# Kernel tuning notes

Hardware: AMD Instinct MI355X
Metric: run time of the kernel (lower is better)

The kernel has to match this reference:

```python
import jax, jax.numpy as jnp
import numpy as np
from jax import lax


def _maxpool_nchw(x, k):
    # Non-overlapping kxk max pool over the last two dims (NCHW).
    return lax.reduce_window(x, -jnp.inf, lax.max,
                             window_dimensions=(1, 1, k, k),
                             window_strides=(1, 1, k, k),
                             padding='VALID')


def setup_inputs() -> dict:
    key = jax.random.key(0)
    k1, k2, k3, k4, k5 = jax.random.split(key, 5)
    B = 16
    return {
        'input_tensor1': jax.random.normal(k1, (B, 128, 48, 48), jnp.float32),
        'input_tensor2': jax.random.normal(k2, (B, 64, 96, 96), jnp.float32),
        'input_tensor3': jax.random.normal(k3, (B, 32, 192, 192), jnp.float32),
        'input_tensor4': jax.random.normal(k4, (B, 16, 384, 384), jnp.float32),
        'pure_ff': jax.random.normal(k5, (B, 256, 24, 24), jnp.float32),
    }


def reference(input_tensor1, input_tensor2, input_tensor3, input_tensor4, pure_ff):
    # and then max-pools. Pooling is per-channel, so this equals pooling once
    # and tiling the pooled result along the channel axis -- same math,
    # without materializing the redundant concat intermediates.
    x1 = jnp.tile(_maxpool_nchw(input_tensor1, 2), (1, 2, 1, 1))   # [B,256,24,24]
    x2 = jnp.tile(_maxpool_nchw(input_tensor2, 4), (1, 4, 1, 1))   # [B,256,24,24]
    x3 = jnp.tile(_maxpool_nchw(input_tensor3, 8), (1, 8, 1, 1))   # [B,256,24,24]
    x4 = jnp.tile(_maxpool_nchw(input_tensor4, 16), (1, 16, 1, 1)) # [B,256,24,24]
    return jax.nn.relu(x1 + x2 + x3 + x4 + pure_ff)
```

## Files before the change

### kernel.cpp

```cpp
#include <hip/hip_runtime.h>
#include <math.h>


namespace {

__device__ __forceinline__ float fmax4(const float4 v) {
  return fmaxf(fmaxf(v.x, v.y), fmaxf(v.z, v.w));
}

__device__ __forceinline__ float4 max4(const float4 a, const float4 b) {
  float4 r;
  r.x = fmaxf(a.x, b.x); r.y = fmaxf(a.y, b.y);
  r.z = fmaxf(a.z, b.z); r.w = fmaxf(a.w, b.w);
  return r;
}

__global__ __launch_bounds__(256, 3) void fused_block(const float* __restrict__ x1,
                                                      const float* __restrict__ x2,
                                                      const float* __restrict__ x3,
                                                      const float* __restrict__ x4,
                                                      const float* __restrict__ ff,
                                                      float* __restrict__ out) {
  __shared__ float s1t[4 * 128];
  __shared__ float s2t[4 * 64];
  __shared__ float s3t[4 * 32];
  __shared__ float s4t[4 * 16];

  const int blk  = blockIdx.x;
  const int b    = blk / 144;
  const int rem  = blk % 144;
  const int oh   = rem / 6;
  const int quad = rem % 6;
  const int tid  = threadIdx.x;


  const size_t o = (size_t)b * 147456 + (size_t)tid * 576 + (size_t)oh * 24 + quad * 4;
  const float4 f = *reinterpret_cast<const float4*>(ff + o);

  const int chA = tid >> 1, pidA = tid & 1;
  const float* pA = x1 + (size_t)b * 294912 + (size_t)chA * 2304
                       + oh * 96 + quad * 8 + pidA * 4;
  const float4 a0 = *reinterpret_cast<const float4*>(pA);
  const float4 a1 = *reinterpret_cast<const float4*>(pA + 48);

  const int chB = tid >> 2, owB = tid & 3;
  const float* pB = x2 + (size_t)b * 589824 + (size_t)chB * 9216
                       + oh * 384 + quad * 16 + owB * 4;
  float4 bv[4];
#pragma unroll
  for (int r = 0; r < 4; ++r) bv[r] = *reinterpret_cast<const float4*>(pB + r * 96);

  const int chC = tid >> 3, owC = (tid >> 1) & 3, hf = tid & 1;
  const float* pC = x3 + (size_t)b * 1179648 + (size_t)chC * 36864
                       + oh * 1536 + quad * 32 + owC * 8 + hf * 4;
  float4 cv[8];
#pragma unroll
  for (int r = 0; r < 8; ++r) cv[r] = *reinterpret_cast<const float4*>(pC + r * 192);

  const int chD = tid >> 4, owD = (tid >> 2) & 3, q = tid & 3;
  const float* pD = x4 + (size_t)b * 2359296 + (size_t)chD * 147456
                       + oh * 6144 + quad * 64 + owD * 16 + q * 4;
  float4 dv[16];
#pragma unroll
  for (int r = 0; r < 16; ++r) dv[r] = *reinterpret_cast<const float4*>(pD + r * 384);


  s1t[(pidA * 2) * 128 + chA]     = fmaxf(fmaxf(a0.x, a0.y), fmaxf(a1.x, a1.y));
  s1t[(pidA * 2 + 1) * 128 + chA] = fmaxf(fmaxf(a0.z, a0.w), fmaxf(a1.z, a1.w));

  {
    const float4 u = max4(max4(bv[0], bv[1]), max4(bv[2], bv[3]));
    s2t[owB * 64 + chB] = fmax4(u);
  }

  {
    const float4 u0 = max4(cv[0], cv[1]), u1 = max4(cv[2], cv[3]);
    const float4 u2 = max4(cv[4], cv[5]), u3 = max4(cv[6], cv[7]);
    float m = fmax4(max4(max4(u0, u1), max4(u2, u3)));
    m = fmaxf(m, __shfl_xor(m, 1));
    if (hf == 0) s3t[owC * 32 + chC] = m;
  }

  {
    float4 t[8];
#pragma unroll
    for (int r = 0; r < 8; ++r) t[r] = max4(dv[r], dv[r + 8]);
    const float4 u0 = max4(t[0], t[1]), u1 = max4(t[2], t[3]);
    const float4 u2 = max4(t[4], t[5]), u3 = max4(t[6], t[7]);
    float m = fmax4(max4(max4(u0, u1), max4(u2, u3)));
    m = fmaxf(m, __shfl_xor(m, 1));
    m = fmaxf(m, __shfl_xor(m, 2));
    if (q == 0) s4t[owD * 16 + chD] = m;
  }

  __syncthreads();

  {
    const int c1 = tid & 127, c2 = tid & 63, c3 = tid & 31, c4 = tid & 15;
    float4 r;
    r.x = fmaxf(s1t[0 * 128 + c1] + s2t[0 * 64 + c2] + s3t[0 * 32 + c3] + s4t[0 * 16 + c4] + f.x, 0.0f);
    r.y = fmaxf(s1t[1 * 128 + c1] + s2t[1 * 64 + c2] + s3t[1 * 32 + c3] + s4t[1 * 16 + c4] + f.y, 0.0f);
    r.z = fmaxf(s1t[2 * 128 + c1] + s2t[2 * 64 + c2] + s3t[2 * 32 + c3] + s4t[2 * 16 + c4] + f.z, 0.0f);
    r.w = fmaxf(s1t[3 * 128 + c1] + s2t[3 * 64 + c2] + s3t[3 * 32 + c3] + s4t[3 * 16 + c4] + f.w, 0.0f);
    *reinterpret_cast<float4*>(out + o) = r;
  }
}

}

extern "C" void kernel_launch(void* const* d_in, const int* in_sizes, int n_in,
                              void* d_out, int out_size, void* d_ws, size_t ws_size,
                              hipStream_t stream) {
  const float* x1 = (const float*)d_in[0];
  const float* x2 = (const float*)d_in[1];
  const float* x3 = (const float*)d_in[2];
  const float* x4 = (const float*)d_in[3];
  const float* ff = (const float*)d_in[4];
  float* out = (float*)d_out;
  (void)d_ws; (void)ws_size; (void)in_sizes; (void)n_in; (void)out_size;

  fused_block<<<2304, 256, 0, stream>>>(x1, x2, x3, x4, ff, out);
}
```

Baseline: 316.5 us.

## Use persistent blocks with double-buffered direct global-to-LDS DMA loads

Replaces the one-shot 2304-block kernel with 256 persistent 512-thread blocks. Each block walks 18 tiles, prefetching the next tile's inputs into a double-buffered LDS region with global_load_lds while it reduces the current tile. The aim is to overlap memory latency with compute and to avoid staging loads through registers. In exchange, tiles shrink to two output columns, so output stores become scalar and poorly coalesced. Occupancy also drops to one large block per CU, with extra barriers and manual vmcnt waits.

```diff
diff --git a/kernel.cpp b/kernel.cpp
--- a/kernel.cpp
+++ b/kernel.cpp
@@ -1,13 +1,37 @@
 #include <hip/hip_runtime.h>
+#include <stdint.h>
 #include <math.h>
 
 
 namespace {
 
+__device__ __forceinline__ void dma16(const float* g, float* l) {
+  __builtin_amdgcn_global_load_lds(
+      (const __attribute__((address_space(1))) uint32_t*)(const void*)g,
+      (__attribute__((address_space(3))) uint32_t*)(void*)l, 16, 0, 0);
+}
+__device__ __forceinline__ void dma4(const float* g, float* l) {
+  __builtin_amdgcn_global_load_lds(
+      (const __attribute__((address_space(1))) uint32_t*)(const void*)g,
+      (__attribute__((address_space(3))) uint32_t*)(void*)l, 4, 0, 0);
+}
+
+#define WAITV(n)                                                \
+  do {                                                          \
+    asm volatile("s_waitcnt vmcnt(" #n ")" ::: "memory");       \
+    __builtin_amdgcn_sched_barrier(0);                          \
+  } while (0)
+
+#define BARRIER()                                               \
+  do {                                                          \
+    asm volatile("" ::: "memory");                              \
+    __builtin_amdgcn_s_barrier();                               \
+    asm volatile("" ::: "memory");                              \
+  } while (0)
+
 __device__ __forceinline__ float fmax4(const float4 v) {
   return fmaxf(fmaxf(v.x, v.y), fmaxf(v.z, v.w));
 }
-
 __device__ __forceinline__ float4 max4(const float4 a, const float4 b) {
   float4 r;
   r.x = fmaxf(a.x, b.x); r.y = fmaxf(a.y, b.y);
@@ -15,94 +39,124 @@
   return r;
 }
 
-__global__ __launch_bounds__(256, 3) void fused_block(const float* __restrict__ x1,
-                                                      const float* __restrict__ x2,
-                                                      const float* __restrict__ x3,
-                                                      const float* __restrict__ x4,
-                                                      const float* __restrict__ ff,
-                                                      float* __restrict__ out) {
-  __shared__ float s1t[4 * 128];
-  __shared__ float s2t[4 * 64];
-  __shared__ float s3t[4 * 32];
-  __shared__ float s4t[4 * 16];
+__global__ __launch_bounds__(512, 1) void fused_dma(const float* __restrict__ x1,
+                                                    const float* __restrict__ x2,
+                                                    const float* __restrict__ x3,
+                                                    const float* __restrict__ x4,
+                                                    const float* __restrict__ ffp,
+                                                    float* __restrict__ out) {
+  __shared__ float buf[2][15360];
+  __shared__ float ffl[2][512];
+  __shared__ float s1t[2 * 128];
+  __shared__ float s2t[2 * 64];
+  __shared__ float s3t[2 * 32];
+  __shared__ float s4t[2 * 16];
 
-  const int blk  = blockIdx.x;
-  const int b    = blk / 144;
-  const int rem  = blk % 144;
-  const int oh   = rem / 6;
-  const int quad = rem % 6;
+  const int cid  = blockIdx.x;
   const int tid  = threadIdx.x;
+  const int wv   = tid >> 6;
+  const int lane = tid & 63;
 
+  auto stage = [&](int tt, int bi) {
+    const int b = tt / 288, rem = tt % 288, oh = rem / 12, cp = rem % 12;
+    const size_t bA = (size_t)b * 294912  + oh * 96   + cp * 4;
+    const size_t bB = (size_t)b * 589824  + oh * 384  + cp * 8;
+    const size_t bC = (size_t)b * 1179648 + oh * 1536 + cp * 16;
+    const size_t bD = (size_t)b * 2359296 + oh * 6144 + cp * 32;
+    const size_t bF = (size_t)b * 147456  + oh * 24   + cp * 2;
+    {
+      const int j = wv * 64 + lane;
+      dma4(ffp + bF + (size_t)(j >> 1) * 576 + (j & 1), &ffl[bi][wv * 64]);
+    }
+    for (int s = wv; s < 60; s += 8) {
+      const float* g;
+      if (s < 4) {
+        const int i = s * 64 + lane;
+        g = x1 + bA + (size_t)(i >> 1) * 2304 + (i & 1) * 48;
+      } else if (s < 12) {
+        const int i = (s - 4) * 64 + lane;
+        g = x2 + bB + (size_t)(i >> 3) * 9216 + ((i >> 1) & 3) * 96 + (i & 1) * 4;
+      } else if (s < 28) {
+        const int i = (s - 12) * 64 + lane;
+        g = x3 + bC + (size_t)(i >> 5) * 36864 + ((i >> 2) & 7) * 192 + (i & 3) * 4;
+      } else {
+        const int i = (s - 28) * 64 + lane;
+        g = x4 + bD + (size_t)(i >> 7) * 147456 + ((i >> 3) & 15) * 384 + (i & 7) * 4;
+      }
+      dma16(g, &buf[bi][s * 256]);
+    }
+  };
 
-  const size_t o = (size_t)b * 147456 + (size_t)tid * 576 + (size_t)oh * 24 + quad * 4;
-  const float4 f = *reinterpret_cast<const float4*>(ff + o);
+  stage(cid, 0);
 
-  const int chA = tid >> 1, pidA = tid & 1;
-  const float* pA = x1 + (size_t)b * 294912 + (size_t)chA * 2304
-                       + oh * 96 + quad * 8 + pidA * 4;
-  const float4 a0 = *reinterpret_cast<const float4*>(pA);
-  const float4 a1 = *reinterpret_cast<const float4*>(pA + 48);
+  for (int i = 0; i < 18; ++i) {
+    const int t   = i * 256 + cid;
+    const int cur = i & 1;
+    const int b = t / 288, rem = t % 288, oh = rem / 12, cp = rem % 12;
 
-  const int chB = tid >> 2, owB = tid & 3;
-  const float* pB = x2 + (size_t)b * 589824 + (size_t)chB * 9216
-                       + oh * 384 + quad * 16 + owB * 4;
-  float4 bv[4];
+    if (i < 17) stage(t + 256, cur ^ 1);
+
+    if (i < 17) {
+      if (wv < 4) WAITV(9); else WAITV(8);
+    } else {
+      WAITV(0);
+    }
+    BARRIER();
+
+    {
+      const float* Bv = &buf[cur][0];
+      if (tid < 256) {
+        const int ch = tid >> 1, w = tid & 1;
+        const float2 r0 = *reinterpret_cast<const float2*>(&Bv[ch * 8 + w * 2]);
+        const float2 r1 = *reinterpret_cast<const float2*>(&Bv[ch * 8 + 4 + w * 2]);
+        s1t[w * 128 + ch] = fmaxf(fmaxf(r0.x, r0.y), fmaxf(r1.x, r1.y));
+      } else if (tid < 384) {
+        const int j = tid - 256, ch = j >> 1, w = j & 1;
+        const float* p = &Bv[1024 + ch * 32 + w * 4];
+        float4 m = *reinterpret_cast<const float4*>(p);
+        m = max4(m, *reinterpret_cast<const float4*>(p + 8));
+        m = max4(m, *reinterpret_cast<const float4*>(p + 16));
+        m = max4(m, *reinterpret_cast<const float4*>(p + 24));
+        s2t[w * 64 + ch] = fmax4(m);
+      } else {
+        const int j = tid - 384, ch = j >> 2, w = (j >> 1) & 1, hf = j & 1;
+        const float* p = &Bv[3072 + ch * 128 + w * 8 + hf * 4];
+        float4 m = *reinterpret_cast<const float4*>(p);
 #pragma unroll
-  for (int r = 0; r < 4; ++r) bv[r] = *reinterpret_cast<const float4*>(pB + r * 96);
+        for (int r = 1; r < 8; ++r)
+          m = max4(m, *reinterpret_cast<const float4*>(p + r * 16));
+        float mm = fmax4(m);
+        mm = fmaxf(mm, __shfl_xor(mm, 1));
+        if (hf == 0) s3t[w * 32 + ch] = mm;
+      }
+      if (tid < 128) {
+        const int ch = tid >> 3, w = (tid >> 2) & 1, q = tid & 3;
+        const float* p = &Bv[7168 + ch * 512 + w * 16 + q * 4];
+        float4 m = *reinterpret_cast<const float4*>(p);
+#pragma unroll
+        for (int r = 1; r < 16; ++r)
+          m = max4(m, *reinterpret_cast<const float4*>(p + r * 32));
+        float mm = fmax4(m);
+        mm = fmaxf(mm, __shfl_xor(mm, 1));
+        mm = fmaxf(mm, __shfl_xor(mm, 2));
+        if (q == 0) s4t[w * 16 + ch] = mm;
+      }
+    }
 
-  const int chC = tid >> 3, owC = (tid >> 1) & 3, hf = tid & 1;
-  const float* pC = x3 + (size_t)b * 1179648 + (size_t)chC * 36864
-                       + oh * 1536 + quad * 32 + owC * 8 + hf * 4;
-  float4 cv[8];
-#pragma unroll
-  for (int r = 0; r < 8; ++r) cv[r] = *reinterpret_cast<const float4*>(pC + r * 192);
+    asm volatile("s_waitcnt lgkmcnt(0)" ::: "memory");
+    __builtin_amdgcn_sched_barrier(0);
+    BARRIER();
 
-  const int chD = tid >> 4, owD = (tid >> 2) & 3, q = tid & 3;
-  const float* pD = x4 + (size_t)b * 2359296 + (size_t)chD * 147456
-                       + oh * 6144 + quad * 64 + owD * 16 + q * 4;
-  float4 dv[16];
-#pragma unroll
-  for (int r = 0; r < 16; ++r) dv[r] = *reinterpret_cast<const float4*>(pD + r * 384);
+    {
+      const int c = tid >> 1, w = tid & 1;
+      float v = s1t[w * 128 + (c & 127)] + s2t[w * 64 + (c & 63)]
+              + s3t[w * 32 + (c & 31)]  + s4t[w * 16 + (c & 15)]
+              + ffl[cur][tid];
+      out[(size_t)b * 147456 + (size_t)c * 576 + oh * 24 + cp * 2 + w] =
+          fmaxf(v, 0.0f);
+    }
 
-
-  s1t[(pidA * 2) * 128 + chA]     = fmaxf(fmaxf(a0.x, a0.y), fmaxf(a1.x, a1.y));
-  s1t[(pidA * 2 + 1) * 128 + chA] = fmaxf(fmaxf(a0.z, a0.w), fmaxf(a1.z, a1.w));
-
-  {
-    const float4 u = max4(max4(bv[0], bv[1]), max4(bv[2], bv[3]));
-    s2t[owB * 64 + chB] = fmax4(u);
-  }
-
-  {
-    const float4 u0 = max4(cv[0], cv[1]), u1 = max4(cv[2], cv[3]);
-    const float4 u2 = max4(cv[4], cv[5]), u3 = max4(cv[6], cv[7]);
-    float m = fmax4(max4(max4(u0, u1), max4(u2, u3)));
-    m = fmaxf(m, __shfl_xor(m, 1));
-    if (hf == 0) s3t[owC * 32 + chC] = m;
-  }
-
-  {
-    float4 t[8];
-#pragma unroll
-    for (int r = 0; r < 8; ++r) t[r] = max4(dv[r], dv[r + 8]);
-    const float4 u0 = max4(t[0], t[1]), u1 = max4(t[2], t[3]);
-    const float4 u2 = max4(t[4], t[5]), u3 = max4(t[6], t[7]);
-    float m = fmax4(max4(max4(u0, u1), max4(u2, u3)));
-    m = fmaxf(m, __shfl_xor(m, 1));
-    m = fmaxf(m, __shfl_xor(m, 2));
-    if (q == 0) s4t[owD * 16 + chD] = m;
-  }
-
-  __syncthreads();
-
-  {
-    const int c1 = tid & 127, c2 = tid & 63, c3 = tid & 31, c4 = tid & 15;
-    float4 r;
-    r.x = fmaxf(s1t[0 * 128 + c1] + s2t[0 * 64 + c2] + s3t[0 * 32 + c3] + s4t[0 * 16 + c4] + f.x, 0.0f);
-    r.y = fmaxf(s1t[1 * 128 + c1] + s2t[1 * 64 + c2] + s3t[1 * 32 + c3] + s4t[1 * 16 + c4] + f.y, 0.0f);
-    r.z = fmaxf(s1t[2 * 128 + c1] + s2t[2 * 64 + c2] + s3t[2 * 32 + c3] + s4t[2 * 16 + c4] + f.z, 0.0f);
-    r.w = fmaxf(s1t[3 * 128 + c1] + s2t[3 * 64 + c2] + s3t[3 * 32 + c3] + s4t[3 * 16 + c4] + f.w, 0.0f);
-    *reinterpret_cast<float4*>(out + o) = r;
+    BARRIER();
   }
 }
 
@@ -119,5 +173,5 @@
   float* out = (float*)d_out;
   (void)d_ws; (void)ws_size; (void)in_sizes; (void)n_in; (void)out_size;
 
-  fused_block<<<2304, 256, 0, stream>>>(x1, x2, x3, x4, ff, out);
+  fused_dma<<<256, 512, 0, stream>>>(x1, x2, x3, x4, ff, out);
 }
```

Result: slower. 326.2 us (+3.0%).
